# Kernel optimization log

Measured on AMD Instinct MI355X. Metric: run time of the kernel, lower is better.

Reference implementation:

```python
import jax, jax.numpy as jnp
import numpy as np

NUM_HEADS = 12


def _rel_pos_table(q_size, k_size, rel_pos):
    # rel_pos: (2*q_size-1, head_dim); q_size == k_size here so no interpolation.
    q_coords = jnp.arange(q_size)[:, None] * max(k_size / q_size, 1.0)
    k_coords = jnp.arange(k_size)[None, :] * max(q_size / k_size, 1.0)
    rel = (q_coords - k_coords + (k_size - 1) * max(q_size / k_size, 1.0)).astype(jnp.int32)
    return rel_pos[rel]  # (q_size, k_size, head_dim)


def setup_inputs() -> dict:
    key = jax.random.key(0)
    ks = jax.random.split(key, 7)
    B, H, W, D = 1, 64, 64, 768
    hd = D // NUM_HEADS
    x = jax.random.normal(ks[0], (B, H, W, D), dtype=jnp.float32)
    w_qkv = jax.random.normal(ks[1], (3 * D, D), dtype=jnp.float32) * (1.0 / np.sqrt(D))
    b_qkv = jnp.zeros((3 * D,), dtype=jnp.float32)
    w_proj = jax.random.normal(ks[2], (D, D), dtype=jnp.float32) * (1.0 / np.sqrt(D))
    b_proj = jnp.zeros((D,), dtype=jnp.float32)
    rel_pos_h = jax.random.normal(ks[3], (2 * H - 1, hd), dtype=jnp.float32) * 0.02
    rel_pos_w = jax.random.normal(ks[4], (2 * W - 1, hd), dtype=jnp.float32) * 0.02
    return {"x": x, "w_qkv": w_qkv, "b_qkv": b_qkv, "w_proj": w_proj,
            "b_proj": b_proj, "rel_pos_h": rel_pos_h, "rel_pos_w": rel_pos_w}


def reference(x, w_qkv, b_qkv, w_proj, b_proj, rel_pos_h, rel_pos_w):
    b, h, w, d = x.shape
    nh = NUM_HEADS
    hd = d // nh
    scale = hd ** -0.5
    # combined qkv projection: (b,h,w,3d) -> (3, b*nh, h*w, hd)
    qkv = x @ w_qkv.T + b_qkv
    qkv = qkv.reshape(b, h * w, 3, nh, hd).transpose(2, 0, 3, 1, 4)
    qkv = qkv.reshape(3, b * nh, h * w, hd)
    q, k, v = qkv[0], qkv[1], qkv[2]
    attn = (q * scale) @ k.swapaxes(-2, -1)  # (b*nh, hw, hw)
    # decomposed 2D relative position bias
    rh = _rel_pos_table(h, h, rel_pos_h)  # (h, h, hd)
    rw = _rel_pos_table(w, w, rel_pos_w)  # (w, w, hd)
    r_q = q.reshape(b * nh, h, w, hd)
    rel_h = jnp.einsum('bhwc,hkc->bhwk', r_q, rh)
    rel_w = jnp.einsum('bhwc,wkc->bhwk', r_q, rw)
    attn = (attn.reshape(b * nh, h, w, h, w)
            + rel_h[:, :, :, :, None]
            + rel_w[:, :, :, None, :]).reshape(b * nh, h * w, h * w)
    attn = jax.nn.softmax(attn, axis=-1)
    out = attn @ v  # (b*nh, hw, hd)
    out = out.reshape(b, nh, h, w, hd).transpose(0, 2, 3, 1, 4).reshape(b, h, w, d)
    return out @ w_proj.T + b_proj
```

## Files before the change

kernel.cpp:

```cpp
#include <hip/hip_runtime.h>
#include <hip/hip_bf16.h>
#include <stdint.h>


typedef unsigned short u16;
typedef unsigned int   u32;
typedef __attribute__((ext_vector_type(8))) short s8v;
typedef __attribute__((ext_vector_type(4))) float f4v;
typedef __attribute__((ext_vector_type(4))) unsigned short us4;
typedef __attribute__((ext_vector_type(8))) unsigned short us8;
typedef __attribute__((ext_vector_type(2))) unsigned int u32x2;

#define DEVI static __device__ __forceinline__

constexpr int   NTOK   = 4096;
constexpr int   DM     = 768;
constexpr float LOG2E_F = 1.4426950408889634f;
constexpr float KSCALE  = 0.18033688011112042f;

#if __has_builtin(__builtin_amdgcn_exp2f)
#define EXP2(x) __builtin_amdgcn_exp2f(x)
#else
#define EXP2(x) exp2f(x)
#endif

DEVI u16 f2bf(float x){
  u32 u = __builtin_bit_cast(u32, x);
  u32 r = (u + 0x7FFFu + ((u >> 16) & 1u)) >> 16;
  return (u16)r;
}
DEVI float bf2f(u16 h){
  u32 u = ((u32)h) << 16;
  return __builtin_bit_cast(float, u);
}
DEVI u32 cvtpk(float lo, float hi){
  u32 r;
  asm("v_cvt_pk_bf16_f32 %0, %1, %2" : "=v"(r) : "v"(lo), "v"(hi));
  return r;
}

typedef const __attribute__((address_space(1))) u32* gp1;
typedef __attribute__((address_space(3))) u32* lp3;
DEVI void gload_lds16(const void* g, void* l){
  __builtin_amdgcn_global_load_lds((gp1)g, (lp3)l, 16, 0, 0);
}

DEVI f4v MFMA16(s8v a, s8v b, f4v c){
  return __builtin_amdgcn_mfma_f32_16x16x32_bf16(a, b, c, 0, 0, 0);
}

DEVI void hard_barrier(){
  __builtin_amdgcn_sched_barrier(0);
  asm volatile("" ::: "memory");
  __builtin_amdgcn_s_barrier();
  asm volatile("" ::: "memory");
  __builtin_amdgcn_sched_barrier(0);
}

__global__ void k_split(const float* __restrict__ in, u16* __restrict__ hi,
                        u16* __restrict__ lo, int n4){
  int i = blockIdx.x * blockDim.x + threadIdx.x;
  int stride = gridDim.x * blockDim.x;
  for (; i < n4; i += stride){
    f4v v = ((const f4v*)in)[i];
    us4 h, l;
#pragma unroll
    for (int j = 0; j < 4; ++j){
      u16 hb = f2bf(v[j]);
      h[j] = hb;
      l[j] = f2bf(v[j] - bf2f(hb));
    }
    ((us4*)hi)[i] = h;
    ((us4*)lo)[i] = l;
  }
}

template<int EPI>
__global__ __launch_bounds__(256)
void k_gemm(const u16* __restrict__ Ah, const u16* __restrict__ Al,
            const u16* __restrict__ Bh, const u16* __restrict__ Bl,
            const float* __restrict__ bias, int K,
            u16* __restrict__ Qh, u16* __restrict__ Ql,
            u16* __restrict__ Kh, u16* __restrict__ Kl,
            float* __restrict__ Vf, float* __restrict__ Cout)
{
  __shared__ __align__(16) unsigned char sm[65536];
  const int t = threadIdx.x;
  const int lane = t & 63, wid = t >> 6;
  const int l15 = lane & 15, g = lane >> 4;
  const int wr = wid >> 1, wc = wid & 1;
  const int m0 = blockIdx.y * 128, n0 = blockIdx.x * 128;

  const char* aGh[2]; const char* aGl[2]; const char* bGh[2]; const char* bGl[2];
#pragma unroll
  for (int ch = 0; ch < 2; ++ch){
    int p = ch * 4096 + t * 16;
    int pair = p >> 7, w = p & 127;
    int u = w ^ ((pair & 7) << 4);
    int row = 2 * pair + (u >> 6);
    int cb  = u & 63;
    aGh[ch] = (const char*)Ah + (size_t)(m0 + row) * K * 2 + cb;
    aGl[ch] = (const char*)Al + (size_t)(m0 + row) * K * 2 + cb;
    bGh[ch] = (const char*)Bh + (size_t)(n0 + row) * K * 2 + cb;
    bGl[ch] = (const char*)Bl + (size_t)(n0 + row) * K * 2 + cb;
  }
  const int axor = ((l15 & 1) * 64 + g * 16) ^ (((l15 >> 1) & 7) << 4);
  const int abase = (wr * 32 + (l15 >> 1)) * 128 + axor;
  const int bbase = 16384 + (wc * 32 + (l15 >> 1)) * 128 + axor;

#pragma unroll
  for (int ch = 0; ch < 2; ++ch){
    gload_lds16(aGh[ch], sm + 0     + ch*4096 + wid*1024);
    gload_lds16(aGl[ch], sm + 8192  + ch*4096 + wid*1024);
    gload_lds16(bGh[ch], sm + 16384 + ch*4096 + wid*1024);
    gload_lds16(bGl[ch], sm + 24576 + ch*4096 + wid*1024);
    aGh[ch] += 64; aGl[ch] += 64; bGh[ch] += 64; bGl[ch] += 64;
  }

  f4v acc[4][4] = {};
  const int KSTEPS = K >> 5;
  for (int kt = 0; kt < KSTEPS; ++kt){
    const int bb = (kt & 1) * 32768;
    if (kt + 1 < KSTEPS){
      const int nb = ((kt + 1) & 1) * 32768;
#pragma unroll
      for (int ch = 0; ch < 2; ++ch){
        gload_lds16(aGh[ch], sm + nb + 0     + ch*4096 + wid*1024);
        gload_lds16(aGl[ch], sm + nb + 8192  + ch*4096 + wid*1024);
        gload_lds16(bGh[ch], sm + nb + 16384 + ch*4096 + wid*1024);
        gload_lds16(bGl[ch], sm + nb + 24576 + ch*4096 + wid*1024);
        aGh[ch] += 64; aGl[ch] += 64; bGh[ch] += 64; bGl[ch] += 64;
      }
      asm volatile("s_waitcnt vmcnt(8)" ::: "memory");
    } else {
      asm volatile("s_waitcnt vmcnt(0)" ::: "memory");
    }
    hard_barrier();

    s8v af[4][2];
#pragma unroll
    for (int mi = 0; mi < 4; ++mi){
      af[mi][0] = *(const s8v*)(sm + bb + abase + mi*1024);
      af[mi][1] = *(const s8v*)(sm + bb + abase + mi*1024 + 8192);
    }
    __builtin_amdgcn_s_setprio(1);
#pragma unroll
    for (int ni = 0; ni < 4; ++ni){
      s8v bh = *(const s8v*)(sm + bb + bbase + ni*1024);
      s8v bl = *(const s8v*)(sm + bb + bbase + ni*1024 + 8192);
#pragma unroll
      for (int mi = 0; mi < 4; ++mi){
        acc[mi][ni] = MFMA16(af[mi][0], bh, acc[mi][ni]);
        acc[mi][ni] = MFMA16(af[mi][0], bl, acc[mi][ni]);
        acc[mi][ni] = MFMA16(af[mi][1], bh, acc[mi][ni]);
      }
    }
    __builtin_amdgcn_s_setprio(0);
    hard_barrier();
  }

  if (EPI == 2){
#pragma unroll
    for (int ni = 0; ni < 4; ++ni){
      int col = n0 + wc*64 + ni*16 + l15;
      float bq = bias[col];
#pragma unroll
      for (int mi = 0; mi < 4; ++mi){
        int rw0 = m0 + wr*64 + mi*16 + g*4;
#pragma unroll
        for (int r = 0; r < 4; ++r)
          Cout[(size_t)(rw0 + r) * DM + col] = acc[mi][ni][r] + bq;
      }
    }
  } else {
#pragma unroll
    for (int ni = 0; ni < 4; ++ni){
      int colb = n0 + wc*64 + ni*16;
      float bq = bias[colb + l15];
      int which = colb / DM;
      int rem   = colb % DM;
      int head  = rem >> 6;
      int c     = (rem & 63) + l15;
#pragma unroll
      for (int mi = 0; mi < 4; ++mi){
        int n = m0 + wr*64 + mi*16 + g*4;
#pragma unroll
        for (int r = 0; r < 4; ++r){
          float v = acc[mi][ni][r] + bq;
          size_t idx = ((size_t)head * NTOK + (n + r)) * 64 + c;
          if (which == 0){
            u16 hb = f2bf(v);
            Qh[idx] = hb; Ql[idx] = f2bf(v - bf2f(hb));
          } else if (which == 1){
            float v2 = v * KSCALE;
            u16 hb = f2bf(v2);
            Kh[idx] = hb; Kl[idx] = f2bf(v2 - bf2f(hb));
          } else {
            Vf[idx] = v;
          }
        }
      }
    }
  }
}

__global__ void k_vtrans(const float* __restrict__ Vf, u16* __restrict__ Vth){
  __shared__ float tile[64][65];
  int h = blockIdx.y, nt = blockIdx.x;
  int t = threadIdx.x;
  {
    int r = t >> 2, c0 = (t & 3) * 16;
    const float* src = Vf + ((size_t)h * NTOK + nt*64 + r) * 64 + c0;
#pragma unroll
    for (int j = 0; j < 4; ++j){
      f4v v = *(const f4v*)(src + j*4);
      tile[r][c0+j*4+0] = v[0]; tile[r][c0+j*4+1] = v[1];
      tile[r][c0+j*4+2] = v[2]; tile[r][c0+j*4+3] = v[3];
    }
  }
  __syncthreads();
  {
    int c = t >> 2, b = (t & 3) * 16;
    us8 o0, o1;
#pragma unroll
    for (int i = 0; i < 16; ++i){
      u16 bv = f2bf(tile[b + i][c]);
      if (i < 8) o0[i] = bv; else o1[i-8] = bv;
    }
    u16* dst = Vth + ((size_t)h * 64 + c) * NTOK + nt*64 + b;
    *(us8*)(dst)     = o0;
    *(us8*)(dst + 8) = o1;
  }
}

__global__ void k_relh(const u16* __restrict__ Qh, const u16* __restrict__ Ql,
                       const float* __restrict__ rp, float* __restrict__ R){
  __shared__ float qs[64][68];
  __shared__ float rs[64][68];
  int h = blockIdx.y, qh = blockIdx.x;
  int t = threadIdx.x;
  {
    int r = t >> 2, c0 = (t & 3) * 16;
    size_t qb = ((size_t)h * NTOK + qh*64 + r) * 64 + c0;
#pragma unroll
    for (int j = 0; j < 2; ++j){
      us8 vh = *(const us8*)(Qh + qb + j*8);
      us8 vl = *(const us8*)(Ql + qb + j*8);
#pragma unroll
      for (int e = 0; e < 8; ++e)
        qs[r][c0 + j*8 + e] = bf2f(vh[e]) + bf2f(vl[e]);
    }
    const float* pr = rp + (size_t)(qh - r + 63) * 64 + c0;
#pragma unroll
    for (int j = 0; j < 4; ++j){
      f4v v = *(const f4v*)(pr + j*4);
      rs[r][c0+j*4+0]=v[0]; rs[r][c0+j*4+1]=v[1];
      rs[r][c0+j*4+2]=v[2]; rs[r][c0+j*4+3]=v[3];
    }
  }
  __syncthreads();
  int qw = t >> 2, k0 = t & 3;
  float acc[16] = {};
  for (int c = 0; c < 64; c += 4){
    f4v qv = *(const f4v*)(&qs[qw][c]);
#pragma unroll
    for (int i = 0; i < 16; ++i){
      f4v rv = *(const f4v*)(&rs[k0 + 4*i][c]);
      acc[i] += qv[0]*rv[0] + qv[1]*rv[1] + qv[2]*rv[2] + qv[3]*rv[3];
    }
  }
  float* o = R + ((size_t)h * NTOK + qh*64 + qw) * 64;
#pragma unroll
  for (int i = 0; i < 16; ++i) o[k0 + 4*i] = acc[i] * LOG2E_F;
}

__global__ void k_relw(const u16* __restrict__ Qh, const u16* __restrict__ Ql,
                       const float* __restrict__ rp, float* __restrict__ R){
  __shared__ float qs[64][68];
  __shared__ float rs[64][68];
  int h = blockIdx.y, qw = blockIdx.x;
  int t = threadIdx.x;
  {
    int r = t >> 2, c0 = (t & 3) * 16;
    size_t qb = ((size_t)h * NTOK + r*64 + qw) * 64 + c0;
#pragma unroll
    for (int j = 0; j < 2; ++j){
      us8 vh = *(const us8*)(Qh + qb + j*8);
      us8 vl = *(const us8*)(Ql + qb + j*8);
#pragma unroll
      for (int e = 0; e < 8; ++e)
        qs[r][c0 + j*8 + e] = bf2f(vh[e]) + bf2f(vl[e]);
    }
    const float* pr = rp + (size_t)(qw - r + 63) * 64 + c0;
#pragma unroll
    for (int j = 0; j < 4; ++j){
      f4v v = *(const f4v*)(pr + j*4);
      rs[r][c0+j*4+0]=v[0]; rs[r][c0+j*4+1]=v[1];
      rs[r][c0+j*4+2]=v[2]; rs[r][c0+j*4+3]=v[3];
    }
  }
  __syncthreads();
  int qh = t >> 2, k0 = t & 3;
  float acc[16] = {};
  for (int c = 0; c < 64; c += 4){
    f4v qv = *(const f4v*)(&qs[qh][c]);
#pragma unroll
    for (int i = 0; i < 16; ++i){
      f4v rv = *(const f4v*)(&rs[k0 + 4*i][c]);
      acc[i] += qv[0]*rv[0] + qv[1]*rv[1] + qv[2]*rv[2] + qv[3]*rv[3];
    }
  }
  float* o = R + ((size_t)h * NTOK + qh*64 + qw) * 64;
#pragma unroll
  for (int i = 0; i < 16; ++i) o[k0 + 4*i] = acc[i] * LOG2E_F;
}

__global__ __launch_bounds__(256)
void k_attn(const u16* __restrict__ Qh, const u16* __restrict__ Ql,
            const u16* __restrict__ Kh, const u16* __restrict__ Kl,
            const u16* __restrict__ Vth,
            const float* __restrict__ Rh, const float* __restrict__ Rw,
            u16* __restrict__ Oh, u16* __restrict__ Ol)
{
  __shared__ __align__(16) unsigned char sm[33792];
  const int t = threadIdx.x;
  const int lane = t & 63, wid = t >> 6;
  const int l15 = lane & 15, g = lane >> 4;
  const int h = blockIdx.y;
  const int qrow0 = blockIdx.x * 64 + wid * 16;

  const char* kGh[2]; const char* kGl[2]; const char* vG[2];
#pragma unroll
  for (int ch = 0; ch < 2; ++ch){
    int p = ch * 4096 + t * 16;
    int row = p >> 7;
    int cb  = (p & 127) ^ ((row & 7) << 4);
    kGh[ch] = (const char*)Kh + ((size_t)h * NTOK + row) * 128 + cb;
    kGl[ch] = (const char*)Kl + ((size_t)h * NTOK + row) * 128 + cb;
    vG[ch]  = (const char*)Vth + ((size_t)h * 64 + row) * (NTOK*2) + cb;
  }

  const size_t qoff = ((size_t)h * NTOK + qrow0 + l15) * 64 + g * 8;
  s8v qh0 = *(const s8v*)(Qh + qoff);
  s8v qh1 = *(const s8v*)(Qh + qoff + 32);
  s8v ql0 = *(const s8v*)(Ql + qoff);
  s8v ql1 = *(const s8v*)(Ql + qoff + 32);

  const int xr  = (l15 & 7) << 4;
  const int kb0 = l15 * 128 + ((g * 16)      ^ xr);
  const int kb1 = l15 * 128 + ((g * 16 + 64) ^ xr);
  const int vb0 = 16384 + kb0;
  const int vb1 = 16384 + kb1;
  const int pbase = 24576 + wid * 2304 + l15 * 144;

  const float* rwp = Rw + ((size_t)h * NTOK + qrow0 + l15) * 64 + 4*g;
  f4v rwv[4];
#pragma unroll
  for (int tt = 0; tt < 4; ++tt) rwv[tt] = *(const f4v*)(rwp + 16*tt);
  const float* rhp = Rh + ((size_t)h * NTOK + qrow0 + l15) * 64;

  f4v st[6];
  auto do_loads = [&](){
    st[0] = *(const f4v*)kGh[0]; st[1] = *(const f4v*)kGh[1];
    st[2] = *(const f4v*)kGl[0]; st[3] = *(const f4v*)kGl[1];
    st[4] = *(const f4v*)vG[0];  st[5] = *(const f4v*)vG[1];
    kGh[0] += 8192; kGh[1] += 8192;
    kGl[0] += 8192; kGl[1] += 8192;
    vG[0]  += 128;  vG[1]  += 128;
  };
  auto do_writes = [&](){
    *(f4v*)(sm + 0     +    0 + t*16) = st[0];
    *(f4v*)(sm + 0     + 4096 + t*16) = st[1];
    *(f4v*)(sm + 8192  +    0 + t*16) = st[2];
    *(f4v*)(sm + 8192  + 4096 + t*16) = st[3];
    *(f4v*)(sm + 16384 +    0 + t*16) = st[4];
    *(f4v*)(sm + 16384 + 4096 + t*16) = st[5];
  };

  do_loads();
  do_writes();
  do_loads();
  asm volatile("s_waitcnt lgkmcnt(0)" ::: "memory");
  hard_barrier();

  f4v o[4] = {};
  float m2 = -1.0e30f, ls = 0.f;

  for (int it = 0; it < 64; ++it){
    const float rhv = rhp[it];

    f4v s[4];
    __builtin_amdgcn_s_setprio(1);
#pragma unroll
    for (int tt = 0; tt < 4; ++tt){
      s8v kh_0 = *(const s8v*)(sm + kb0 + tt*2048);
      s8v kh_1 = *(const s8v*)(sm + kb1 + tt*2048);
      s8v kl_0 = *(const s8v*)(sm + kb0 + tt*2048 + 8192);
      s8v kl_1 = *(const s8v*)(sm + kb1 + tt*2048 + 8192);
      f4v a = {};
      a = MFMA16(kh_0, qh0, a);
      a = MFMA16(kh_1, qh1, a);
      a = MFMA16(kl_0, qh0, a);
      a = MFMA16(kl_1, qh1, a);
      a = MFMA16(kh_0, ql0, a);
      a = MFMA16(kh_1, ql1, a);
      s[tt] = a;
    }
    __builtin_amdgcn_s_setprio(0);

    float pm = -1.0e30f;
#pragma unroll
    for (int tt = 0; tt < 4; ++tt){
#pragma unroll
      for (int r = 0; r < 4; ++r){
        s[tt][r] += rhv + rwv[tt][r];
        pm = fmaxf(pm, s[tt][r]);
      }
    }
    pm = fmaxf(pm, __shfl_xor(pm, 16, 64));
    pm = fmaxf(pm, __shfl_xor(pm, 32, 64));
    const float mn = fmaxf(m2, pm);
    const float fr = EXP2(m2 - mn);
    m2 = mn;
    float ps = 0.f;
#pragma unroll
    for (int tt = 0; tt < 4; ++tt){
#pragma unroll
      for (int r = 0; r < 4; ++r){
        float p = EXP2(s[tt][r] - m2);
        s[tt][r] = p;
        ps += p;
      }
    }
    ps += __shfl_xor(ps, 16, 64);
    ps += __shfl_xor(ps, 32, 64);
    ls = ls * fr + ps;

#pragma unroll
    for (int tt = 0; tt < 4; ++tt){
      u32x2 w2;
      w2[0] = cvtpk(s[tt][0], s[tt][1]);
      w2[1] = cvtpk(s[tt][2], s[tt][3]);
      *(u32x2*)(sm + pbase + 8*g + 32*tt) = w2;
    }
#pragma unroll
    for (int dt = 0; dt < 4; ++dt){
#pragma unroll
      for (int r = 0; r < 4; ++r) o[dt][r] *= fr;
    }
    s8v pa0 = *(const s8v*)(sm + pbase + 16*g);
    s8v pa1 = *(const s8v*)(sm + pbase + 16*g + 64);
    __builtin_amdgcn_s_setprio(1);
#pragma unroll
    for (int dt = 0; dt < 4; ++dt){
      s8v v0 = *(const s8v*)(sm + vb0 + dt*2048);
      s8v v1 = *(const s8v*)(sm + vb1 + dt*2048);
      o[dt] = MFMA16(v0, pa0, o[dt]);
      o[dt] = MFMA16(v1, pa1, o[dt]);
    }
    __builtin_amdgcn_s_setprio(0);

    hard_barrier();
    if (it < 63){
      do_writes();
      if (it < 62) do_loads();
    }
    asm volatile("s_waitcnt lgkmcnt(0)" ::: "memory");
    hard_barrier();
  }

  const float inv = 1.0f / ls;
  const size_t obase = (size_t)(qrow0 + l15) * DM + h*64 + 4*g;
#pragma unroll
  for (int dt = 0; dt < 4; ++dt){
    us4 hv, lv;
#pragma unroll
    for (int r = 0; r < 4; ++r){
      float v = o[dt][r] * inv;
      u16 hb = f2bf(v);
      hv[r] = hb;
      lv[r] = f2bf(v - bf2f(hb));
    }
    *(us4*)(Oh + obase + 16*dt) = hv;
    *(us4*)(Ol + obase + 16*dt) = lv;
  }
}

extern "C" void kernel_launch(void* const* d_in, const int* in_sizes, int n_in,
                              void* d_out, int out_size, void* d_ws, size_t ws_size,
                              hipStream_t stream){
  (void)in_sizes; (void)n_in; (void)out_size; (void)ws_size;
  const float* x      = (const float*)d_in[0];
  const float* w_qkv  = (const float*)d_in[1];
  const float* b_qkv  = (const float*)d_in[2];
  const float* w_proj = (const float*)d_in[3];
  const float* b_proj = (const float*)d_in[4];
  const float* rph    = (const float*)d_in[5];
  const float* rpw    = (const float*)d_in[6];
  float* out = (float*)d_out;

  char* w = (char*)d_ws;
  size_t off = 0;
  auto nxt = [&](size_t b) -> char* {
    char* p = w + off; off += (b + 255) & ~(size_t)255; return p;
  };
  u16*   Xh  = (u16*)  nxt((size_t)NTOK*DM*2);
  u16*   Xl  = (u16*)  nxt((size_t)NTOK*DM*2);
  u16*   Wqh = (u16*)  nxt((size_t)3*DM*DM*2);
  u16*   Wql = (u16*)  nxt((size_t)3*DM*DM*2);
  u16*   Wph = (u16*)  nxt((size_t)DM*DM*2);
  u16*   Wpl = (u16*)  nxt((size_t)DM*DM*2);
  u16*   Qh  = (u16*)  nxt((size_t)NTOK*DM*2);
  u16*   Ql  = (u16*)  nxt((size_t)NTOK*DM*2);
  u16*   Kh  = (u16*)  nxt((size_t)NTOK*DM*2);
  u16*   Kl  = (u16*)  nxt((size_t)NTOK*DM*2);
  float* Vf  = (float*)nxt((size_t)NTOK*DM*4);
  u16*   Vth = (u16*)  nxt((size_t)NTOK*DM*2);
  float* Rh  = (float*)nxt((size_t)12*NTOK*64*4);
  float* Rw  = (float*)nxt((size_t)12*NTOK*64*4);
  u16*   Oh  = Xh;
  u16*   Ol  = Xl;

  k_split<<<dim3(3072), dim3(256), 0, stream>>>(x,      Xh,  Xl,  NTOK*DM/4);
  k_split<<<dim3(1728), dim3(256), 0, stream>>>(w_qkv,  Wqh, Wql, 3*DM*DM/4);
  k_split<<<dim3(576),  dim3(256), 0, stream>>>(w_proj, Wph, Wpl, DM*DM/4);

  k_gemm<1><<<dim3(18, 32), dim3(256), 0, stream>>>(
      Xh, Xl, Wqh, Wql, b_qkv, DM, Qh, Ql, Kh, Kl, Vf, nullptr);

  k_vtrans<<<dim3(64, 12), dim3(256), 0, stream>>>(Vf, Vth);
  k_relh  <<<dim3(64, 12), dim3(256), 0, stream>>>(Qh, Ql, rph, Rh);
  k_relw  <<<dim3(64, 12), dim3(256), 0, stream>>>(Qh, Ql, rpw, Rw);

  k_attn<<<dim3(64, 12), dim3(256), 0, stream>>>(Qh, Ql, Kh, Kl, Vth, Rh, Rw, Oh, Ol);

  k_gemm<2><<<dim3(6, 32), dim3(256), 0, stream>>>(
      Oh, Ol, Wph, Wpl, b_proj, DM,
      nullptr, nullptr, nullptr, nullptr, nullptr, out);
}
```

Baseline: 348.1 us.

## Split attention waves 2x2 over query and key halves with split-softmax merge

```diff
diff --git a/kernel.cpp b/kernel.cpp
--- a/kernel.cpp
+++ b/kernel.cpp
@@ -322,12 +322,14 @@
             const float* __restrict__ Rh, const float* __restrict__ Rw,
             u16* __restrict__ Oh, u16* __restrict__ Ol)
 {
-  __shared__ __align__(16) unsigned char sm[33792];
+  __shared__ __align__(16) unsigned char sm[34816];
   const int t = threadIdx.x;
   const int lane = t & 63, wid = t >> 6;
   const int l15 = lane & 15, g = lane >> 4;
   const int h = blockIdx.y;
-  const int qrow0 = blockIdx.x * 64 + wid * 16;
+  const int qh_w = wid & 1;
+  const int kh_w = wid >> 1;
+  const int qtile = blockIdx.x * 64;
 
   const char* kGh[2]; const char* kGl[2]; const char* vG[2];
 #pragma unroll
@@ -340,24 +342,42 @@
     vG[ch]  = (const char*)Vth + ((size_t)h * 64 + row) * (NTOK*2) + cb;
   }
 
-  const size_t qoff = ((size_t)h * NTOK + qrow0 + l15) * 64 + g * 8;
-  s8v qh0 = *(const s8v*)(Qh + qoff);
-  s8v qh1 = *(const s8v*)(Qh + qoff + 32);
-  s8v ql0 = *(const s8v*)(Ql + qoff);
-  s8v ql1 = *(const s8v*)(Ql + qoff + 32);
-
-  const int xr  = (l15 & 7) << 4;
-  const int kb0 = l15 * 128 + ((g * 16)      ^ xr);
-  const int kb1 = l15 * 128 + ((g * 16 + 64) ^ xr);
-  const int vb0 = 16384 + kb0;
-  const int vb1 = 16384 + kb1;
-  const int pbase = 24576 + wid * 2304 + l15 * 144;
-
-  const float* rwp = Rw + ((size_t)h * NTOK + qrow0 + l15) * 64 + 4*g;
-  f4v rwv[4];
-#pragma unroll
-  for (int tt = 0; tt < 4; ++tt) rwv[tt] = *(const f4v*)(rwp + 16*tt);
-  const float* rhp = Rh + ((size_t)h * NTOK + qrow0 + l15) * 64;
+  s8v qfh[2][2], qfl[2][2];
+#pragma unroll
+  for (int qg = 0; qg < 2; ++qg){
+    const size_t qoff =
+      ((size_t)h * NTOK + qtile + qh_w*32 + qg*16 + l15) * 64 + g * 8;
+    qfh[qg][0] = *(const s8v*)(Qh + qoff);
+    qfh[qg][1] = *(const s8v*)(Qh + qoff + 32);
+    qfl[qg][0] = *(const s8v*)(Ql + qoff);
+    qfl[qg][1] = *(const s8v*)(Ql + qoff + 32);
+  }
+
+  const int xr = (l15 & 7) << 4;
+  int kb[2][2];
+#pragma unroll
+  for (int kg = 0; kg < 2; ++kg){
+    int rl = kh_w*32 + kg*16 + l15;
+    kb[kg][0] = rl*128 + ((g*16)      ^ xr);
+    kb[kg][1] = rl*128 + ((g*16 + 64) ^ xr);
+  }
+  int vb[4];
+#pragma unroll
+  for (int dt = 0; dt < 4; ++dt)
+    vb[dt] = 16384 + (dt*16 + l15)*128 + ((kh_w*64 + g*16) ^ xr);
+
+  const int preg = 24576 + wid * 2560;
+
+  f4v rwv[2][2];
+  const float* rhp[2];
+#pragma unroll
+  for (int qg = 0; qg < 2; ++qg){
+    int q = qtile + qh_w*32 + qg*16 + l15;
+    const float* base = Rw + ((size_t)h * NTOK + q) * 64 + kh_w*32 + 4*g;
+    rwv[0][qg] = *(const f4v*)(base);
+    rwv[1][qg] = *(const f4v*)(base + 16);
+    rhp[qg] = Rh + ((size_t)h * NTOK + q) * 64;
+  }
 
   f4v st[6];
   auto do_loads = [&](){
@@ -383,80 +403,106 @@
   asm volatile("s_waitcnt lgkmcnt(0)" ::: "memory");
   hard_barrier();
 
-  f4v o[4] = {};
-  float m2 = -1.0e30f, ls = 0.f;
+  f4v o[4][2] = {};
+  float m2[2] = {-1.0e30f, -1.0e30f}, ls[2] = {0.f, 0.f};
 
   for (int it = 0; it < 64; ++it){
-    const float rhv = rhp[it];
-
-    f4v s[4];
+    float rhv[2];
+    rhv[0] = rhp[0][it];
+    rhv[1] = rhp[1][it];
+
+    f4v s[2][2];
     __builtin_amdgcn_s_setprio(1);
 #pragma unroll
-    for (int tt = 0; tt < 4; ++tt){
-      s8v kh_0 = *(const s8v*)(sm + kb0 + tt*2048);
-      s8v kh_1 = *(const s8v*)(sm + kb1 + tt*2048);
-      s8v kl_0 = *(const s8v*)(sm + kb0 + tt*2048 + 8192);
-      s8v kl_1 = *(const s8v*)(sm + kb1 + tt*2048 + 8192);
-      f4v a = {};
-      a = MFMA16(kh_0, qh0, a);
-      a = MFMA16(kh_1, qh1, a);
-      a = MFMA16(kl_0, qh0, a);
-      a = MFMA16(kl_1, qh1, a);
-      a = MFMA16(kh_0, ql0, a);
-      a = MFMA16(kh_1, ql1, a);
-      s[tt] = a;
+    for (int kg = 0; kg < 2; ++kg){
+      s8v kh0 = *(const s8v*)(sm + kb[kg][0]);
+      s8v kh1 = *(const s8v*)(sm + kb[kg][1]);
+      s8v kl0 = *(const s8v*)(sm + kb[kg][0] + 8192);
+      s8v kl1 = *(const s8v*)(sm + kb[kg][1] + 8192);
+#pragma unroll
+      for (int qg = 0; qg < 2; ++qg){
+        f4v a = {};
+        a = MFMA16(kh0, qfh[qg][0], a);
+        a = MFMA16(kh1, qfh[qg][1], a);
+        a = MFMA16(kl0, qfh[qg][0], a);
+        a = MFMA16(kl1, qfh[qg][1], a);
+        a = MFMA16(kh0, qfl[qg][0], a);
+        a = MFMA16(kh1, qfl[qg][1], a);
+        s[kg][qg] = a;
+      }
     }
     __builtin_amdgcn_s_setprio(0);
 
-    float pm = -1.0e30f;
-#pragma unroll
-    for (int tt = 0; tt < 4; ++tt){
-#pragma unroll
-      for (int r = 0; r < 4; ++r){
-        s[tt][r] += rhv + rwv[tt][r];
-        pm = fmaxf(pm, s[tt][r]);
-      }
-    }
-    pm = fmaxf(pm, __shfl_xor(pm, 16, 64));
-    pm = fmaxf(pm, __shfl_xor(pm, 32, 64));
-    const float mn = fmaxf(m2, pm);
-    const float fr = EXP2(m2 - mn);
-    m2 = mn;
-    float ps = 0.f;
-#pragma unroll
-    for (int tt = 0; tt < 4; ++tt){
-#pragma unroll
-      for (int r = 0; r < 4; ++r){
-        float p = EXP2(s[tt][r] - m2);
-        s[tt][r] = p;
-        ps += p;
-      }
-    }
-    ps += __shfl_xor(ps, 16, 64);
-    ps += __shfl_xor(ps, 32, 64);
-    ls = ls * fr + ps;
-
-#pragma unroll
-    for (int tt = 0; tt < 4; ++tt){
-      u32x2 w2;
-      w2[0] = cvtpk(s[tt][0], s[tt][1]);
-      w2[1] = cvtpk(s[tt][2], s[tt][3]);
-      *(u32x2*)(sm + pbase + 8*g + 32*tt) = w2;
+    float pm[2] = {-1.0e30f, -1.0e30f};
+#pragma unroll
+    for (int kg = 0; kg < 2; ++kg){
+#pragma unroll
+      for (int qg = 0; qg < 2; ++qg){
+#pragma unroll
+        for (int r = 0; r < 4; ++r){
+          s[kg][qg][r] += rhv[qg] + rwv[kg][qg][r];
+          pm[qg] = fmaxf(pm[qg], s[kg][qg][r]);
+        }
+      }
+    }
+#pragma unroll
+    for (int qg = 0; qg < 2; ++qg){
+      pm[qg] = fmaxf(pm[qg], __shfl_xor(pm[qg], 16, 64));
+      pm[qg] = fmaxf(pm[qg], __shfl_xor(pm[qg], 32, 64));
+    }
+    float fr[2];
+#pragma unroll
+    for (int qg = 0; qg < 2; ++qg){
+      float mn = fmaxf(m2[qg], pm[qg]);
+      fr[qg] = EXP2(m2[qg] - mn);
+      m2[qg] = mn;
+    }
+    float ps[2] = {0.f, 0.f};
+#pragma unroll
+    for (int kg = 0; kg < 2; ++kg){
+#pragma unroll
+      for (int qg = 0; qg < 2; ++qg){
+#pragma unroll
+        for (int r = 0; r < 4; ++r){
+          float p = EXP2(s[kg][qg][r] - m2[qg]);
+          s[kg][qg][r] = p;
+          ps[qg] += p;
+        }
+      }
+    }
+#pragma unroll
+    for (int qg = 0; qg < 2; ++qg){
+      ps[qg] += __shfl_xor(ps[qg], 16, 64);
+      ps[qg] += __shfl_xor(ps[qg], 32, 64);
+      ls[qg] = ls[qg] * fr[qg] + ps[qg];
+    }
+
+#pragma unroll
+    for (int qg = 0; qg < 2; ++qg){
+#pragma unroll
+      for (int kg = 0; kg < 2; ++kg){
+        u32x2 w2;
+        w2[0] = cvtpk(s[kg][qg][0], s[kg][qg][1]);
+        w2[1] = cvtpk(s[kg][qg][2], s[kg][qg][3]);
+        *(u32x2*)(sm + preg + (qg*16 + l15)*80 + kg*32 + 8*g) = w2;
+      }
     }
 #pragma unroll
     for (int dt = 0; dt < 4; ++dt){
 #pragma unroll
-      for (int r = 0; r < 4; ++r) o[dt][r] *= fr;
-    }
-    s8v pa0 = *(const s8v*)(sm + pbase + 16*g);
-    s8v pa1 = *(const s8v*)(sm + pbase + 16*g + 64);
+      for (int qg = 0; qg < 2; ++qg){
+#pragma unroll
+        for (int r = 0; r < 4; ++r) o[dt][qg][r] *= fr[qg];
+      }
+    }
+    s8v pa0 = *(const s8v*)(sm + preg + l15*80        + 16*g);
+    s8v pa1 = *(const s8v*)(sm + preg + (16+l15)*80   + 16*g);
     __builtin_amdgcn_s_setprio(1);
 #pragma unroll
     for (int dt = 0; dt < 4; ++dt){
-      s8v v0 = *(const s8v*)(sm + vb0 + dt*2048);
-      s8v v1 = *(const s8v*)(sm + vb1 + dt*2048);
-      o[dt] = MFMA16(v0, pa0, o[dt]);
-      o[dt] = MFMA16(v1, pa1, o[dt]);
+      s8v vf = *(const s8v*)(sm + vb[dt]);
+      o[dt][0] = MFMA16(vf, pa0, o[dt][0]);
+      o[dt][1] = MFMA16(vf, pa1, o[dt][1]);
     }
     __builtin_amdgcn_s_setprio(0);
 
@@ -469,20 +515,51 @@
     hard_barrier();
   }
 
-  const float inv = 1.0f / ls;
-  const size_t obase = (size_t)(qrow0 + l15) * DM + h*64 + 4*g;
-#pragma unroll
-  for (int dt = 0; dt < 4; ++dt){
-    us4 hv, lv;
-#pragma unroll
-    for (int r = 0; r < 4; ++r){
-      float v = o[dt][r] * inv;
-      u16 hb = f2bf(v);
-      hv[r] = hb;
-      lv[r] = f2bf(v - bf2f(hb));
-    }
-    *(us4*)(Oh + obase + 16*dt) = hv;
-    *(us4*)(Ol + obase + 16*dt) = lv;
+  if (kh_w == 1){
+#pragma unroll
+    for (int qg = 0; qg < 2; ++qg){
+#pragma unroll
+      for (int dt = 0; dt < 4; ++dt)
+        *(f4v*)(sm + qh_w*8704 + (qg*16 + l15)*272 + dt*64 + 16*g) = o[dt][qg];
+      if (g == 0){
+        *(float*)(sm + 17408 + qh_w*256 + (qg*16 + l15)*8)     = m2[qg];
+        *(float*)(sm + 17408 + qh_w*256 + (qg*16 + l15)*8 + 4) = ls[qg];
+      }
+    }
+  }
+  asm volatile("s_waitcnt lgkmcnt(0)" ::: "memory");
+  hard_barrier();
+  if (kh_w == 0){
+    float ai[2], bi[2];
+#pragma unroll
+    for (int qg = 0; qg < 2; ++qg){
+      float mp = *(const float*)(sm + 17408 + qh_w*256 + (qg*16 + l15)*8);
+      float lp = *(const float*)(sm + 17408 + qh_w*256 + (qg*16 + l15)*8 + 4);
+      float M  = fmaxf(m2[qg], mp);
+      float a  = EXP2(m2[qg] - M);
+      float b  = EXP2(mp - M);
+      float inv = 1.0f / (a*ls[qg] + b*lp);
+      ai[qg] = a * inv; bi[qg] = b * inv;
+    }
+#pragma unroll
+    for (int qg = 0; qg < 2; ++qg){
+      const size_t obase =
+        (size_t)(qtile + qh_w*32 + qg*16 + l15) * DM + h*64 + 4*g;
+#pragma unroll
+      for (int dt = 0; dt < 4; ++dt){
+        f4v op = *(const f4v*)(sm + qh_w*8704 + (qg*16 + l15)*272 + dt*64 + 16*g);
+        us4 hv, lv;
+#pragma unroll
+        for (int r = 0; r < 4; ++r){
+          float v = o[dt][qg][r] * ai[qg] + op[r] * bi[qg];
+          u16 hb = f2bf(v);
+          hv[r] = hb;
+          lv[r] = f2bf(v - bf2f(hb));
+        }
+        *(us4*)(Oh + obase + 16*dt) = hv;
+        *(us4*)(Ol + obase + 16*dt) = lv;
+      }
+    }
   }
 }
 
```

Measured after the change: 394.6 us. 13.4% more time.
